# Kernel optimization log

Hardware: AMD Instinct MI355X
Metric: run time of the kernel (lower is better)

Reference implementation:

```python
import jax, jax.numpy as jnp
import numpy as np

N_NODES = 50000
N_EDGES = 800000
NODE_IN = 16
EDGE_IN = 3
G_DIM = 8
LATENT = 128
NODE_OUT = 1
EDGE_OUT = 1


def _dense_init(key, fan_in, fan_out):
    # flax default: lecun_normal weights, zero bias
    w = jax.random.normal(key, (fan_in, fan_out), jnp.float32) / jnp.sqrt(float(fan_in))
    b = jnp.zeros((fan_out,), jnp.float32)
    return w, b


def setup_inputs() -> dict:
    key = jax.random.key(0)
    ks = jax.random.split(key, 12)
    nodes = jax.random.normal(ks[0], (N_NODES, NODE_IN), jnp.float32)
    edges = jax.random.normal(ks[1], (N_EDGES, EDGE_IN), jnp.float32)
    globals_ = jax.random.normal(ks[2], (1, G_DIM), jnp.float32)
    senders = jax.random.randint(ks[3], (N_EDGES,), 0, N_NODES, jnp.int32)
    receivers = jax.random.randint(ks[4], (N_EDGES,), 0, N_NODES, jnp.int32)
    W_en, b_en = _dense_init(ks[5], NODE_IN, LATENT)      # encoder node Dense
    W_ee, b_ee = _dense_init(ks[6], EDGE_IN, LATENT)      # encoder edge Dense
    mlp_in = 3 * LATENT + G_DIM                           # concat(nodes, sent, recv, globals)
    W1, b1 = _dense_init(ks[7], mlp_in, LATENT)           # node MLP layer 1 (relu)
    W2, b2 = _dense_init(ks[8], LATENT, LATENT)           # node MLP layer 2
    W_dn, b_dn = _dense_init(ks[9], LATENT, NODE_OUT)     # decoder node Dense
    W_de, b_de = _dense_init(ks[10], LATENT, EDGE_OUT)    # decoder edge Dense
    return dict(nodes=nodes, edges=edges, globals_=globals_, senders=senders,
                receivers=receivers, W_en=W_en, b_en=b_en, W_ee=W_ee, b_ee=b_ee,
                W1=W1, b1=b1, W2=W2, b2=b2, W_dn=W_dn, b_dn=b_dn, W_de=W_de, b_de=b_de)


def reference(nodes, edges, globals_, senders, receivers,
              W_en, b_en, W_ee, b_ee, W1, b1, W2, b2, W_dn, b_dn, W_de, b_de):
    n = nodes.shape[0]
    # Encoder (GraphMapFeatures)
    h_n = nodes @ W_en + b_en                     # [N, L]
    h_e = edges @ W_ee + b_ee                     # [E, L]
    # One jraph.GraphNetwork step, update_edge_fn=None -> edges unchanged.
    # sent/received aggregation = segment_sum of edge features by sender/receiver.
    sent = jax.ops.segment_sum(h_e, senders, num_segments=n)      # [N, L]
    recv = jax.ops.segment_sum(h_e, receivers, num_segments=n)    # [N, L]
    gbc = jnp.broadcast_to(globals_[0], (n, globals_.shape[1]))   # single graph
    x = jnp.concatenate((h_n, sent, recv, gbc), axis=1)           # [N, 3L+G]
    x = jax.nn.relu(x @ W1 + b1)
    h_n = x @ W2 + b2
    # update_global_fn reconstructs concat([time], static) == globals (identity).
    # Decoder
    nodes_out = h_n @ W_dn + b_dn                 # [N, 1]
    edges_out = h_e @ W_de + b_de                 # [E, 1]
    return nodes_out, edges_out
```

## Files before the change

### kernel.cpp

```cpp
#include <hip/hip_runtime.h>

#define N_NODES 50000
#define N_EDGES 800000

#define ESR_OFF    0
#define CONSTS_OFF 400000
#define SCAL_OFF   404096
#define PART_OFF   404608

#define NBINS      13
#define BINSZ      4000
#define MAX_CHUNKS 20

__global__ void precompute_kernel(
    const float* __restrict__ g,
    const float* __restrict__ W_en,
    const float* __restrict__ b_en,
    const float* __restrict__ W_ee,
    const float* __restrict__ b_ee,
    const float* __restrict__ W1,
    const float* __restrict__ b1,
    const float* __restrict__ W2,
    const float* __restrict__ b2,
    const float* __restrict__ W_dn,
    const float* __restrict__ b_dn,
    const float* __restrict__ W_de,
    const float* __restrict__ b_de,
    float* __restrict__ ws)
{
    const int s = blockIdx.x;
    const int k = threadIdx.x;
    float* consts = ws + CONSTS_OFF;
    float* scal   = ws + SCAL_OFF;

    if (s < 16) {
        float acc = 0.f;
        for (int l = 0; l < 128; ++l)
            acc += W_en[s * 128 + l] * W1[l * 128 + k];
        consts[k * 32 + s] = acc;
    } else if (s < 19) {
        const int j = s - 16;
        float acc = 0.f;
        for (int l = 0; l < 128; ++l)
            acc += W_ee[j * 128 + l] * W1[(128 + l) * 128 + k];
        consts[k * 32 + s] = acc;
    } else if (s < 22) {
        const int j = s - 19;
        float acc = 0.f;
        for (int l = 0; l < 128; ++l)
            acc += W_ee[j * 128 + l] * W1[(256 + l) * 128 + k];
        consts[k * 32 + s] = acc;
    } else if (s == 22) {
        float acc = b1[k];
        for (int l = 0; l < 128; ++l)
            acc += b_en[l] * W1[l * 128 + k];
        for (int j = 0; j < 8; ++j)
            acc += g[j] * W1[(384 + j) * 128 + k];
        consts[k * 32 + 22] = acc;
    } else if (s == 23) {
        float acc = 0.f;
        for (int l = 0; l < 128; ++l)
            acc += b_ee[l] * W1[(128 + l) * 128 + k];
        consts[k * 32 + 23] = acc;
    } else if (s == 24) {
        float acc = 0.f;
        for (int l = 0; l < 128; ++l)
            acc += b_ee[l] * W1[(256 + l) * 128 + k];
        consts[k * 32 + 24] = acc;
    } else if (s == 25) {
        float acc = 0.f;
        for (int j = 0; j < 128; ++j)
            acc += W2[k * 128 + j] * W_dn[j];
        consts[k * 32 + 25] = acc;
        consts[k * 32 + 26] = 0.f;
        consts[k * 32 + 27] = 0.f;
    } else {
        if (k == 0) {
            float c = b_dn[0];
            for (int j = 0; j < 128; ++j) c += b2[j] * W_dn[j];
            scal[0] = c;
            float ce = b_de[0];
            for (int l = 0; l < 128; ++l) ce += b_ee[l] * W_de[l];
            scal[1] = ce;
            scal[5] = 0.f; scal[6] = 0.f; scal[7] = 0.f;
        }
        if (k < 3) {
            float acc = 0.f;
            for (int l = 0; l < 128; ++l)
                acc += W_ee[k * 128 + l] * W_de[l];
            scal[2 + k] = acc;
        }
    }
}

__global__ __launch_bounds__(256) void edge_out_kernel(
    const float* __restrict__ edges,
    const float* __restrict__ ws,
    float* __restrict__ out_edges)
{
    const int e4 = (blockIdx.x * 256 + threadIdx.x) * 4;
    if (e4 >= N_EDGES) return;
    const float* scal = ws + SCAL_OFF;
    const float w0 = scal[2], w1 = scal[3], w2 = scal[4], cb = scal[1];
    const float4* ep = (const float4*)(edges + (size_t)e4 * 3);
    const float4 f0 = ep[0], f1 = ep[1], f2 = ep[2];
    float4 o;
    o.x = fmaf(f0.x, w0, fmaf(f0.y, w1, fmaf(f0.z, w2, cb)));
    o.y = fmaf(f0.w, w0, fmaf(f1.x, w1, fmaf(f1.y, w2, cb)));
    o.z = fmaf(f1.z, w0, fmaf(f1.w, w1, fmaf(f2.x, w2, cb)));
    o.w = fmaf(f2.y, w0, fmaf(f2.z, w1, fmaf(f2.w, w2, cb)));
    *(float4*)(out_edges + e4) = o;
}

__global__ __launch_bounds__(512) void agg_kernel(
    const float* __restrict__ edges,
    const int*   __restrict__ senders,
    const int*   __restrict__ receivers,
    float* __restrict__ part_s,
    float* __restrict__ part_r,
    int ce)
{
    __shared__ float4 acc4[BINSZ];
    float* acc = (float*)acc4;
    const int tid = threadIdx.x;
    for (int i = tid; i < BINSZ; i += 512)
        acc4[i] = make_float4(0.f, 0.f, 0.f, 0.f);
    __syncthreads();

    const int chunk  = blockIdx.x;
    const int binid  = blockIdx.y;
    const bool is_s  = binid < NBINS;
    const int bin    = is_s ? binid : binid - NBINS;
    const int lo     = bin * BINSZ;
    const int* __restrict__ idx = is_s ? senders : receivers;

    const int e_beg = chunk * ce;
    const int e_end = min(e_beg + ce, N_EDGES);
    for (int e8 = e_beg + tid * 8; e8 < e_end; e8 += 512 * 8) {
        const int4 ia = *(const int4*)(idx + e8);
        const int4 ib = *(const int4*)(idx + e8 + 4);
        const unsigned d0 = (unsigned)(ia.x - lo), d1 = (unsigned)(ia.y - lo);
        const unsigned d2 = (unsigned)(ia.z - lo), d3 = (unsigned)(ia.w - lo);
        const unsigned d4 = (unsigned)(ib.x - lo), d5 = (unsigned)(ib.y - lo);
        const unsigned d6 = (unsigned)(ib.z - lo), d7 = (unsigned)(ib.w - lo);
        if ((d0 < BINSZ) | (d1 < BINSZ) | (d2 < BINSZ) | (d3 < BINSZ)) {
            const float4* ep = (const float4*)(edges + (size_t)e8 * 3);
            const float4 f0 = ep[0], f1 = ep[1], f2 = ep[2];
            if (d0 < BINSZ) {
                atomicAdd(&acc[d0 * 4 + 0], f0.x); atomicAdd(&acc[d0 * 4 + 1], f0.y);
                atomicAdd(&acc[d0 * 4 + 2], f0.z); atomicAdd(&acc[d0 * 4 + 3], 1.0f);
            }
            if (d1 < BINSZ) {
                atomicAdd(&acc[d1 * 4 + 0], f0.w); atomicAdd(&acc[d1 * 4 + 1], f1.x);
                atomicAdd(&acc[d1 * 4 + 2], f1.y); atomicAdd(&acc[d1 * 4 + 3], 1.0f);
            }
            if (d2 < BINSZ) {
                atomicAdd(&acc[d2 * 4 + 0], f1.z); atomicAdd(&acc[d2 * 4 + 1], f1.w);
                atomicAdd(&acc[d2 * 4 + 2], f2.x); atomicAdd(&acc[d2 * 4 + 3], 1.0f);
            }
            if (d3 < BINSZ) {
                atomicAdd(&acc[d3 * 4 + 0], f2.y); atomicAdd(&acc[d3 * 4 + 1], f2.z);
                atomicAdd(&acc[d3 * 4 + 2], f2.w); atomicAdd(&acc[d3 * 4 + 3], 1.0f);
            }
        }
        if ((d4 < BINSZ) | (d5 < BINSZ) | (d6 < BINSZ) | (d7 < BINSZ)) {
            const float4* ep = (const float4*)(edges + (size_t)e8 * 3 + 12);
            const float4 f0 = ep[0], f1 = ep[1], f2 = ep[2];
            if (d4 < BINSZ) {
                atomicAdd(&acc[d4 * 4 + 0], f0.x); atomicAdd(&acc[d4 * 4 + 1], f0.y);
                atomicAdd(&acc[d4 * 4 + 2], f0.z); atomicAdd(&acc[d4 * 4 + 3], 1.0f);
            }
            if (d5 < BINSZ) {
                atomicAdd(&acc[d5 * 4 + 0], f0.w); atomicAdd(&acc[d5 * 4 + 1], f1.x);
                atomicAdd(&acc[d5 * 4 + 2], f1.y); atomicAdd(&acc[d5 * 4 + 3], 1.0f);
            }
            if (d6 < BINSZ) {
                atomicAdd(&acc[d6 * 4 + 0], f1.z); atomicAdd(&acc[d6 * 4 + 1], f1.w);
                atomicAdd(&acc[d6 * 4 + 2], f2.x); atomicAdd(&acc[d6 * 4 + 3], 1.0f);
            }
            if (d7 < BINSZ) {
                atomicAdd(&acc[d7 * 4 + 0], f2.y); atomicAdd(&acc[d7 * 4 + 1], f2.z);
                atomicAdd(&acc[d7 * 4 + 2], f2.w); atomicAdd(&acc[d7 * 4 + 3], 1.0f);
            }
        }
    }
    __syncthreads();

    float* base = (is_s ? part_s : part_r) + (size_t)chunk * (N_NODES * 4) + (size_t)lo * 4;
    const int lim = min(BINSZ, N_NODES - lo);
    float4* dst = (float4*)base;
    for (int i = tid; i < lim; i += 512)
        dst[i] = acc4[i];
}

__global__ __launch_bounds__(256) void edge_kernel_atomic(
    const float* __restrict__ edges,
    const int*   __restrict__ senders,
    const int*   __restrict__ receivers,
    float* __restrict__ ws)
{
    const int e = blockIdx.x * 256 + threadIdx.x;
    if (e >= N_EDGES) return;
    const float e0 = edges[e * 3 + 0];
    const float e1 = edges[e * 3 + 1];
    const float e2 = edges[e * 3 + 2];
    const int s = senders[e];
    const int r = receivers[e];
    float* esr = ws + ESR_OFF;
    atomicAdd(&esr[s * 8 + 0], e0);
    atomicAdd(&esr[s * 8 + 1], e1);
    atomicAdd(&esr[s * 8 + 2], e2);
    atomicAdd(&esr[s * 8 + 3], 1.0f);
    atomicAdd(&esr[r * 8 + 4], e0);
    atomicAdd(&esr[r * 8 + 5], e1);
    atomicAdd(&esr[r * 8 + 6], e2);
    atomicAdd(&esr[r * 8 + 7], 1.0f);
}

__global__ __launch_bounds__(256) void node_kernel(
    const float* __restrict__ nodes,
    const float* __restrict__ ws,
    const float* __restrict__ part_s,
    const float* __restrict__ part_r,
    float* __restrict__ out_nodes,
    int nchunks)
{
    __shared__ float4 lds4[128 * 8];
    const float4* consts4 = (const float4*)(ws + CONSTS_OFF);
    for (int i = threadIdx.x; i < 128 * 8; i += 256)
        lds4[i] = consts4[i];
    __syncthreads();

    const int n = blockIdx.x * 256 + threadIdx.x;
    if (n >= N_NODES) return;

    const float4* np4 = (const float4*)(nodes + (size_t)n * 16);
    const float4 n0 = np4[0], n1 = np4[1], n2 = np4[2], n3 = np4[3];

    float4 es = make_float4(0.f, 0.f, 0.f, 0.f);
    float4 er = make_float4(0.f, 0.f, 0.f, 0.f);
    if (nchunks > 0) {
        for (int c = 0; c < nchunks; ++c) {
            const float4 a = *(const float4*)(part_s + (size_t)c * (N_NODES * 4) + (size_t)n * 4);
            const float4 b = *(const float4*)(part_r + (size_t)c * (N_NODES * 4) + (size_t)n * 4);
            es.x += a.x; es.y += a.y; es.z += a.z; es.w += a.w;
            er.x += b.x; er.y += b.y; er.z += b.z; er.w += b.w;
        }
    } else {
        const float4* p = (const float4*)(ws + ESR_OFF + (size_t)n * 8);
        es = p[0];
        er = p[1];
    }

    float acc = 0.f;
#pragma unroll 4
    for (int k = 0; k < 128; ++k) {
        const float4* c4 = &lds4[k * 8];
        const float4 m0 = c4[0], m1 = c4[1], m2 = c4[2], m3 = c4[3];
        const float4 q0 = c4[4];
        const float4 q1 = c4[5];
        const float4 q2 = c4[6];
        float pre = q1.z
            + n0.x * m0.x + n0.y * m0.y + n0.z * m0.z + n0.w * m0.w
            + n1.x * m1.x + n1.y * m1.y + n1.z * m1.z + n1.w * m1.w
            + n2.x * m2.x + n2.y * m2.y + n2.z * m2.z + n2.w * m2.w
            + n3.x * m3.x + n3.y * m3.y + n3.z * m3.z + n3.w * m3.w
            + es.x * q0.x + es.y * q0.y + es.z * q0.z
            + er.x * q0.w + er.y * q1.x + er.z * q1.y
            + es.w * q1.w + er.w * q2.x;
        acc += fmaxf(pre, 0.f) * q2.y;
    }
    const float* scal = ws + SCAL_OFF;
    out_nodes[n] = acc + scal[0];
}

extern "C" void kernel_launch(void* const* d_in, const int* in_sizes, int n_in,
                              void* d_out, int out_size, void* d_ws, size_t ws_size,
                              hipStream_t stream) {
    const float* nodes     = (const float*)d_in[0];
    const float* edges     = (const float*)d_in[1];
    const float* globals_  = (const float*)d_in[2];
    const int*   senders   = (const int*)d_in[3];
    const int*   receivers = (const int*)d_in[4];
    const float* W_en = (const float*)d_in[5];
    const float* b_en = (const float*)d_in[6];
    const float* W_ee = (const float*)d_in[7];
    const float* b_ee = (const float*)d_in[8];
    const float* W1   = (const float*)d_in[9];
    const float* b1   = (const float*)d_in[10];
    const float* W2   = (const float*)d_in[11];
    const float* b2   = (const float*)d_in[12];
    const float* W_dn = (const float*)d_in[13];
    const float* b_dn = (const float*)d_in[14];
    const float* W_de = (const float*)d_in[15];
    const float* b_de = (const float*)d_in[16];

    float* ws = (float*)d_ws;
    float* out = (float*)d_out;

    precompute_kernel<<<27, 128, 0, stream>>>(
        globals_, W_en, b_en, W_ee, b_ee, W1, b1, W2, b2,
        W_dn, b_dn, W_de, b_de, ws);

    edge_out_kernel<<<(N_EDGES / 4 + 255) / 256, 256, 0, stream>>>(
        edges, ws, out + N_NODES);

    long ws_floats = (long)(ws_size / 4);
    long per_chunk = 2L * N_NODES * 4;
    long avail = (ws_floats - PART_OFF) / per_chunk;
    int nchunks = (int)(avail < 0 ? 0 : (avail > MAX_CHUNKS ? MAX_CHUNKS : avail));

    float* part_s = ws + PART_OFF;
    float* part_r = part_s + (size_t)nchunks * (N_NODES * 4);

    if (nchunks >= 1) {
        int ce = (N_EDGES + nchunks - 1) / nchunks;
        ce = (ce + 7) & ~7;
        dim3 grid(nchunks, 2 * NBINS);
        agg_kernel<<<grid, 512, 0, stream>>>(
            edges, senders, receivers, part_s, part_r, ce);
    } else {
        hipMemsetAsync(ws + ESR_OFF, 0, (size_t)N_NODES * 8 * sizeof(float), stream);
        edge_kernel_atomic<<<(N_EDGES + 255) / 256, 256, 0, stream>>>(
            edges, senders, receivers, ws);
    }

    node_kernel<<<(N_NODES + 255) / 256, 256, 0, stream>>>(
        nodes, ws, part_s, part_r, out, nchunks);
}
```

Measured before the change: 177.6 us.

## Shrink aggregation bins, prefetch indices, and read node-kernel constants from global memory

Halves the LDS bin size and doubles the number of bins, so each aggregation block uses less shared memory and more blocks fit per CU (with a launch-bounds occupancy hint). It adds software prefetching of the next sender/receiver index vectors, overlapping index loads with the LDS atomics. The node kernel drops its LDS staging of the weight constants, reads them directly from global memory (uniform loads), and uses 64-thread blocks to launch more blocks. The trade-off is that each edge-index stream is re-read by twice as many bins, and the node kernel depends on cache hits for the constants.

```diff
diff --git a/kernel.cpp b/kernel.cpp
--- a/kernel.cpp
+++ b/kernel.cpp
@@ -8,8 +8,8 @@
 #define SCAL_OFF   404096
 #define PART_OFF   404608
 
-#define NBINS      13
-#define BINSZ      4000
+#define NBINS      25
+#define BINSZ      2000
 #define MAX_CHUNKS 20
 
 __global__ void precompute_kernel(
@@ -112,7 +112,7 @@
     *(float4*)(out_edges + e4) = o;
 }
 
-__global__ __launch_bounds__(512) void agg_kernel(
+__global__ __launch_bounds__(512, 8) void agg_kernel(
     const float* __restrict__ edges,
     const int*   __restrict__ senders,
     const int*   __restrict__ receivers,
@@ -136,9 +136,21 @@
 
     const int e_beg = chunk * ce;
     const int e_end = min(e_beg + ce, N_EDGES);
-    for (int e8 = e_beg + tid * 8; e8 < e_end; e8 += 512 * 8) {
-        const int4 ia = *(const int4*)(idx + e8);
-        const int4 ib = *(const int4*)(idx + e8 + 4);
+    const int STRIDE = 512 * 8;
+
+    int e8 = e_beg + tid * 8;
+    int4 ia = make_int4(-1, -1, -1, -1), ib = ia;
+    if (e8 < e_end) {
+        ia = *(const int4*)(idx + e8);
+        ib = *(const int4*)(idx + e8 + 4);
+    }
+    while (e8 < e_end) {
+        const int e8n = e8 + STRIDE;
+        int4 ian = ia, ibn = ib;
+        if (e8n < e_end) {
+            ian = *(const int4*)(idx + e8n);
+            ibn = *(const int4*)(idx + e8n + 4);
+        }
         const unsigned d0 = (unsigned)(ia.x - lo), d1 = (unsigned)(ia.y - lo);
         const unsigned d2 = (unsigned)(ia.z - lo), d3 = (unsigned)(ia.w - lo);
         const unsigned d4 = (unsigned)(ib.x - lo), d5 = (unsigned)(ib.y - lo);
@@ -183,13 +195,14 @@
                 atomicAdd(&acc[d7 * 4 + 2], f2.w); atomicAdd(&acc[d7 * 4 + 3], 1.0f);
             }
         }
+        ia = ian; ib = ibn;
+        e8 = e8n;
     }
     __syncthreads();
 
     float* base = (is_s ? part_s : part_r) + (size_t)chunk * (N_NODES * 4) + (size_t)lo * 4;
-    const int lim = min(BINSZ, N_NODES - lo);
     float4* dst = (float4*)base;
-    for (int i = tid; i < lim; i += 512)
+    for (int i = tid; i < BINSZ; i += 512)
         dst[i] = acc4[i];
 }
 
@@ -217,7 +230,7 @@
     atomicAdd(&esr[r * 8 + 7], 1.0f);
 }
 
-__global__ __launch_bounds__(256) void node_kernel(
+__global__ __launch_bounds__(64) void node_kernel(
     const float* __restrict__ nodes,
     const float* __restrict__ ws,
     const float* __restrict__ part_s,
@@ -225,13 +238,7 @@
     float* __restrict__ out_nodes,
     int nchunks)
 {
-    __shared__ float4 lds4[128 * 8];
-    const float4* consts4 = (const float4*)(ws + CONSTS_OFF);
-    for (int i = threadIdx.x; i < 128 * 8; i += 256)
-        lds4[i] = consts4[i];
-    __syncthreads();
-
-    const int n = blockIdx.x * 256 + threadIdx.x;
+    const int n = blockIdx.x * 64 + threadIdx.x;
     if (n >= N_NODES) return;
 
     const float4* np4 = (const float4*)(nodes + (size_t)n * 16);
@@ -252,14 +259,17 @@
         er = p[1];
     }
 
+    const float* cst = ws + CONSTS_OFF;
     float acc = 0.f;
 #pragma unroll 4
     for (int k = 0; k < 128; ++k) {
-        const float4* c4 = &lds4[k * 8];
-        const float4 m0 = c4[0], m1 = c4[1], m2 = c4[2], m3 = c4[3];
-        const float4 q0 = c4[4];
-        const float4 q1 = c4[5];
-        const float4 q2 = c4[6];
+        const float4 m0 = *(const float4*)(cst + k * 32 + 0);
+        const float4 m1 = *(const float4*)(cst + k * 32 + 4);
+        const float4 m2 = *(const float4*)(cst + k * 32 + 8);
+        const float4 m3 = *(const float4*)(cst + k * 32 + 12);
+        const float4 q0 = *(const float4*)(cst + k * 32 + 16);
+        const float4 q1 = *(const float4*)(cst + k * 32 + 20);
+        const float4 q2 = *(const float4*)(cst + k * 32 + 24);
         float pre = q1.z
             + n0.x * m0.x + n0.y * m0.y + n0.z * m0.z + n0.w * m0.w
             + n1.x * m1.x + n1.y * m1.y + n1.z * m1.z + n1.w * m1.w
@@ -325,6 +335,6 @@
             edges, senders, receivers, ws);
     }
 
-    node_kernel<<<(N_NODES + 255) / 256, 256, 0, stream>>>(
+    node_kernel<<<(N_NODES + 63) / 64, 64, 0, stream>>>(
         nodes, ws, part_s, part_r, out, nchunks);
 }
```

Result: no change. 175.6 us, median of 2 (-1.1%).
